# Optimization experiments

Measured on AMD Instinct MI355X. Metric: run time of the kernel, lower is better.

The kernel has to match this reference:

```python
import jax, jax.numpy as jnp
import numpy as np

B, L, D = 1, 512, 1280


def setup_inputs() -> dict:
    key = jax.random.key(0)
    k1, k2, k3 = jax.random.split(key, 3)
    prev_result = jax.random.normal(k1, (B, L, D), dtype=jnp.float32)
    # nn.Linear(2*D, 2): store weight as [2D, 2] so forward is x @ W + b
    W = jax.random.normal(k2, (2 * D, 2), dtype=jnp.float32) * (1.0 / np.sqrt(2 * D))
    b = jax.random.normal(k3, (2,), dtype=jnp.float32) * 0.01
    return {"prev_result": prev_result, "W": W, "b": b}


def reference(prev_result, W, b):
    # Dropout is identity at inference. The torch code builds
    # pairwise = cat(x_i * x_j, x_i - x_j) of shape [B,L,L,2D] then applies
    # Linear(2D, 2). We fuse: split W into the prod half Wp and diff half Wd.
    Wp, Wd = W[:D], W[D:]                                   # each [D, 2]
    # (x_i * x_j) @ Wp  -- bilinear contraction, no [B,L,L,2D] intermediate
    prod_term = jnp.einsum('bid,bjd,dk->bijk', prev_result, prev_result, Wp)
    # (x_i - x_j) @ Wd = (x @ Wd)_i - (x @ Wd)_j
    d_proj = prev_result @ Wd                                # [B, L, 2]
    diff_term = d_proj[:, :, None, :] - d_proj[:, None, :, :]
    prediction = prod_term + diff_term + b                   # [B, L, L, 2]
    prediction = (prediction + prediction.transpose(0, 2, 1, 3)) / 2
    return prediction[:, 1:-1, 1:-1]                         # [B, L-2, L-2, 2]
```

## Files before the change

kernel.cpp:

```cpp
#include <hip/hip_runtime.h>

#define D_DIM 1280
#define ODIM  510

typedef short bf16x8 __attribute__((ext_vector_type(8)));
typedef float f32x4  __attribute__((ext_vector_type(4)));
typedef unsigned uint4n __attribute__((ext_vector_type(4)));

__device__ __forceinline__ unsigned pkbf(float a, float b) {
  unsigned ua = __float_as_uint(a), ub = __float_as_uint(b);
  return ((ua + 0x8000u) >> 16) | ((ub + 0x8000u) & 0xffff0000u);
}

__global__ __launch_bounds__(256, 1) void pcmd_prep(
    const float* __restrict__ X,
    const float* __restrict__ W,
    unsigned short* __restrict__ Xbf,
    unsigned short* __restrict__ A0,
    unsigned short* __restrict__ A1)
{
  int t = (int)blockIdx.x * 256 + (int)threadIdx.x;
  int r = t / 160;
  int c = t - r * 160;
  const float* px = X + (size_t)r * D_DIM + c * 8;
  float4 x0 = *(const float4*)px;
  float4 x1 = *(const float4*)(px + 4);
  const float* pw = W + (size_t)c * 16;
  float4 w0 = *(const float4*)(pw +  0);
  float4 w1 = *(const float4*)(pw +  4);
  float4 w2 = *(const float4*)(pw +  8);
  float4 w3 = *(const float4*)(pw + 12);
  size_t o = (size_t)r * D_DIM + c * 8;
  uint4n vx, v0, v1;
  vx.x = pkbf(x0.x, x0.y);            vx.y = pkbf(x0.z, x0.w);
  vx.z = pkbf(x1.x, x1.y);            vx.w = pkbf(x1.z, x1.w);
  v0.x = pkbf(x0.x*w0.x, x0.y*w0.z);  v0.y = pkbf(x0.z*w1.x, x0.w*w1.z);
  v0.z = pkbf(x1.x*w2.x, x1.y*w2.z);  v0.w = pkbf(x1.z*w3.x, x1.w*w3.z);
  v1.x = pkbf(x0.x*w0.y, x0.y*w0.w);  v1.y = pkbf(x0.z*w1.y, x0.w*w1.w);
  v1.z = pkbf(x1.x*w2.y, x1.y*w2.w);  v1.w = pkbf(x1.z*w3.y, x1.w*w3.w);
  __builtin_nontemporal_store(vx, (uint4n*)(Xbf + o));
  __builtin_nontemporal_store(v0, (uint4n*)(A0  + o));
  __builtin_nontemporal_store(v1, (uint4n*)(A1  + o));
}

__global__ __launch_bounds__(256, 4) void pcmd_gemm(
    const unsigned short* __restrict__ Xbf,
    const unsigned short* __restrict__ A0,
    const unsigned short* __restrict__ A1,
    const float* __restrict__ b,
    float* __restrict__ out)
{
  __shared__ float sR[4][2][16][16];

  const int tid  = threadIdx.x;
  const int lane = tid & 63;
  const int wv   = tid >> 6;
  const int m    = lane & 15;
  const int quad = lane >> 4;

  const int i_base = 1 + (int)blockIdx.y * 16;
  const int j_base = 1 + (int)blockIdx.x * 16;
  int gi = i_base + m; if (gi > 511) gi = 511;
  int gj = j_base + m; if (gj > 511) gj = 511;

  const int k0 = wv * 320;
  const unsigned short* pa0 = A0  + (size_t)gi * D_DIM + k0 + quad * 8;
  const unsigned short* pa1 = A1  + (size_t)gi * D_DIM + k0 + quad * 8;
  const unsigned short* pb  = Xbf + (size_t)gj * D_DIM + k0 + quad * 8;

  bf16x8 ra0[4], ra1[4], rb[4];
  #pragma unroll
  for (int s = 0; s < 4; ++s) {
    ra0[s] = *(const bf16x8*)(pa0 + s * 32);
    ra1[s] = *(const bf16x8*)(pa1 + s * 32);
    rb[s]  = *(const bf16x8*)(pb  + s * 32);
  }

  f32x4 acc0 = {0.f, 0.f, 0.f, 0.f};
  f32x4 acc1 = {0.f, 0.f, 0.f, 0.f};

  #pragma unroll
  for (int s = 0; s < 10; ++s) {
    int cur = s & 3;
    bf16x8 a0 = ra0[cur], a1 = ra1[cur], bb = rb[cur];
    if (s + 4 < 10) {
      ra0[cur] = *(const bf16x8*)(pa0 + (s + 4) * 32);
      ra1[cur] = *(const bf16x8*)(pa1 + (s + 4) * 32);
      rb[cur]  = *(const bf16x8*)(pb  + (s + 4) * 32);
    }
    acc0 = __builtin_amdgcn_mfma_f32_16x16x32_bf16(a0, bb, acc0, 0, 0, 0);
    acc1 = __builtin_amdgcn_mfma_f32_16x16x32_bf16(a1, bb, acc1, 0, 0, 0);
  }

  #pragma unroll
  for (int r = 0; r < 4; ++r) {
    sR[wv][0][quad * 4 + r][m] = acc0[r];
    sR[wv][1][quad * 4 + r][m] = acc1[r];
  }
  __syncthreads();

  const int il = tid >> 4, jl = tid & 15;
  const int i = i_base + il, j = j_base + jl;
  if (i <= ODIM && j <= ODIM) {
    float2 v;
    v.x = sR[0][0][il][jl] + sR[1][0][il][jl] + sR[2][0][il][jl] + sR[3][0][il][jl] + b[0];
    v.y = sR[0][1][il][jl] + sR[1][1][il][jl] + sR[2][1][il][jl] + sR[3][1][il][jl] + b[1];
    *(float2*)(out + ((size_t)(i - 1) * ODIM + (j - 1)) * 2) = v;
  }
}

extern "C" void kernel_launch(void* const* d_in, const int* in_sizes, int n_in,
                              void* d_out, int out_size, void* d_ws, size_t ws_size,
                              hipStream_t stream) {
  const float* X = (const float*)d_in[0];
  const float* W = (const float*)d_in[1];
  const float* b = (const float*)d_in[2];
  float* out = (float*)d_out;
  (void)in_sizes; (void)n_in; (void)out_size; (void)ws_size;

  const size_t PLANE = (size_t)512 * D_DIM;
  unsigned short* Xbf = (unsigned short*)d_ws;
  unsigned short* A0  = Xbf + PLANE;
  unsigned short* A1  = A0 + PLANE;

  hipLaunchKernelGGL(pcmd_prep, dim3(320), dim3(256), 0, stream, X, W, Xbf, A0, A1);
  hipLaunchKernelGGL(pcmd_gemm, dim3(32, 32), dim3(256), 0, stream, Xbf, A0, A1, b, out);
}
```

Baseline: 77.45 us.

## Exploit output symmetry: compute upper-triangular tiles and mirror-store transposes

The symmetrized output is symmetric in i and j, so the GEMM grid is changed from a full 32x32 tile grid to a 1D launch over the 528 upper-triangular tiles. Each tile index is mapped to (bi, bj) with a sqrt-based inverse and a correction step. Off-diagonal blocks write both their tile and its transpose, read from shared memory. The shared buffer is padded to 17 columns to avoid bank conflicts on the transposed read. The prep kernel's nontemporal stores become plain stores. This roughly halves the MFMA and operand-load work, at the cost of fewer blocks to fill the GPU and a second output write per block.

Result: faster. 73.15 us (-5.6%).

```diff
diff --git a/kernel.cpp b/kernel.cpp
--- a/kernel.cpp
+++ b/kernel.cpp
@@ -1,11 +1,11 @@
 #include <hip/hip_runtime.h>
+#include <math.h>
 
 #define D_DIM 1280
 #define ODIM  510
 
 typedef short bf16x8 __attribute__((ext_vector_type(8)));
 typedef float f32x4  __attribute__((ext_vector_type(4)));
-typedef unsigned uint4n __attribute__((ext_vector_type(4)));
 
 __device__ __forceinline__ unsigned pkbf(float a, float b) {
   unsigned ua = __float_as_uint(a), ub = __float_as_uint(b);
@@ -31,16 +31,16 @@
   float4 w2 = *(const float4*)(pw +  8);
   float4 w3 = *(const float4*)(pw + 12);
   size_t o = (size_t)r * D_DIM + c * 8;
-  uint4n vx, v0, v1;
+  uint4 vx, v0, v1;
   vx.x = pkbf(x0.x, x0.y);            vx.y = pkbf(x0.z, x0.w);
   vx.z = pkbf(x1.x, x1.y);            vx.w = pkbf(x1.z, x1.w);
   v0.x = pkbf(x0.x*w0.x, x0.y*w0.z);  v0.y = pkbf(x0.z*w1.x, x0.w*w1.z);
   v0.z = pkbf(x1.x*w2.x, x1.y*w2.z);  v0.w = pkbf(x1.z*w3.x, x1.w*w3.z);
   v1.x = pkbf(x0.x*w0.y, x0.y*w0.w);  v1.y = pkbf(x0.z*w1.y, x0.w*w1.w);
   v1.z = pkbf(x1.x*w2.y, x1.y*w2.w);  v1.w = pkbf(x1.z*w3.y, x1.w*w3.w);
-  __builtin_nontemporal_store(vx, (uint4n*)(Xbf + o));
-  __builtin_nontemporal_store(v0, (uint4n*)(A0  + o));
-  __builtin_nontemporal_store(v1, (uint4n*)(A1  + o));
+  *(uint4*)(Xbf + o) = vx;
+  *(uint4*)(A0  + o) = v0;
+  *(uint4*)(A1  + o) = v1;
 }
 
 __global__ __launch_bounds__(256, 4) void pcmd_gemm(
@@ -50,7 +50,20 @@
     const float* __restrict__ b,
     float* __restrict__ out)
 {
-  __shared__ float sR[4][2][16][16];
+  __shared__ float sR[4][2][16][17];
+
+  const int t = (int)blockIdx.x;
+  int bi = (int)((65.0 - sqrt(4225.0 - 8.0 * (double)t)) * 0.5);
+  {
+    int s0 = bi * 32 - (bi * (bi - 1)) / 2;
+    if (t < s0) { --bi; s0 = bi * 32 - (bi * (bi - 1)) / 2; }
+    int s1 = (bi + 1) * 32 - ((bi + 1) * bi) / 2;
+    if (t >= s1) { ++bi; s0 = s1; }
+    s0 = bi * 32 - (bi * (bi - 1)) / 2;
+    bi = bi;
+  }
+  const int start = bi * 32 - (bi * (bi - 1)) / 2;
+  const int bj = bi + (t - start);
 
   const int tid  = threadIdx.x;
   const int lane = tid & 63;
@@ -58,8 +71,8 @@
   const int m    = lane & 15;
   const int quad = lane >> 4;
 
-  const int i_base = 1 + (int)blockIdx.y * 16;
-  const int j_base = 1 + (int)blockIdx.x * 16;
+  const int i_base = 1 + bi * 16;
+  const int j_base = 1 + bj * 16;
   int gi = i_base + m; if (gi > 511) gi = 511;
   int gj = j_base + m; if (gj > 511) gj = 511;
 
@@ -99,13 +112,27 @@
   }
   __syncthreads();
 
+  const float b0 = b[0], b1 = b[1];
   const int il = tid >> 4, jl = tid & 15;
-  const int i = i_base + il, j = j_base + jl;
-  if (i <= ODIM && j <= ODIM) {
-    float2 v;
-    v.x = sR[0][0][il][jl] + sR[1][0][il][jl] + sR[2][0][il][jl] + sR[3][0][il][jl] + b[0];
-    v.y = sR[0][1][il][jl] + sR[1][1][il][jl] + sR[2][1][il][jl] + sR[3][1][il][jl] + b[1];
-    *(float2*)(out + ((size_t)(i - 1) * ODIM + (j - 1)) * 2) = v;
+
+  {
+    const int i = i_base + il, j = j_base + jl;
+    if (i <= ODIM && j <= ODIM) {
+      float2 v;
+      v.x = sR[0][0][il][jl] + sR[1][0][il][jl] + sR[2][0][il][jl] + sR[3][0][il][jl] + b0;
+      v.y = sR[0][1][il][jl] + sR[1][1][il][jl] + sR[2][1][il][jl] + sR[3][1][il][jl] + b1;
+      *(float2*)(out + ((size_t)(i - 1) * ODIM + (j - 1)) * 2) = v;
+    }
+  }
+
+  if (bi != bj) {
+    const int i = j_base + il, j = i_base + jl;
+    if (i <= ODIM && j <= ODIM) {
+      float2 v;
+      v.x = sR[0][0][jl][il] + sR[1][0][jl][il] + sR[2][0][jl][il] + sR[3][0][jl][il] + b0;
+      v.y = sR[0][1][jl][il] + sR[1][1][jl][il] + sR[2][1][jl][il] + sR[3][1][jl][il] + b1;
+      *(float2*)(out + ((size_t)(i - 1) * ODIM + (j - 1)) * 2) = v;
+    }
   }
 }
 
@@ -124,5 +151,5 @@
   unsigned short* A1  = A0 + PLANE;
 
   hipLaunchKernelGGL(pcmd_prep, dim3(320), dim3(256), 0, stream, X, W, Xbf, A0, A1);
-  hipLaunchKernelGGL(pcmd_gemm, dim3(32, 32), dim3(256), 0, stream, Xbf, A0, A1, b, out);
+  hipLaunchKernelGGL(pcmd_gemm, dim3(528), dim3(256), 0, stream, Xbf, A0, A1, b, out);
 }
```
